# Kernel tuning notes

Measured on AMD Instinct MI355X. Metric: run time of the kernel, lower is better.

Reference implementation:

```python
import jax, jax.numpy as jnp
import numpy as np

N = 10000      # nodes
E = 160000     # edges
C = 72         # hidden dim = 18 * mul (mul=4)
A = 16         # node_attr dim (16x0e)
L = 3          # layers
O = 64         # output dim (64x0e)
B = 16         # graphs in batch
IN_DIM = 18    # irreps_node_input dim
SH = 9         # spherical harmonics dim, lmax=2
FC = 100       # radial MLP hidden (fc_neurons=[1,100])
MAX_RADIUS = 2.0
NUM_NEIGHBORS = 16.0
NUM_NODES = 625.0


def sph_harm_l2(d):
    # component-normalized real spherical harmonics up to l=2 on unit vectors d [E,3]
    x, y, z = d[:, 0], d[:, 1], d[:, 2]
    s3, s5, s15 = 3.0 ** 0.5, 5.0 ** 0.5, 15.0 ** 0.5
    return jnp.stack([
        jnp.ones_like(x),
        s3 * x, s3 * y, s3 * z,
        s15 * x * y, s15 * y * z, (s5 / 2.0) * (3.0 * z * z - 1.0),
        s15 * x * z, (s15 / 2.0) * (x * x - y * y),
    ], axis=1)  # [E, 9]


def setup_inputs() -> dict:
    key = jax.random.key(0)
    ks = jax.random.split(key, 16)
    pos = jax.random.normal(ks[0], (N, 3), dtype=jnp.float32)
    node_attr = jax.random.normal(ks[1], (N, A), dtype=jnp.float32)
    batch = jnp.sort(jax.random.randint(ks[2], (N,), 0, B))
    edge_src = jax.random.randint(ks[3], (E,), 0, N)
    edge_dst = jax.random.randint(ks[4], (E,), 0, N)
    W_in = jax.random.normal(ks[5], (IN_DIM, C), dtype=jnp.float32) / np.sqrt(IN_DIM)
    W_tp = jax.random.normal(ks[6], (L, SH, C, C), dtype=jnp.float32) / np.sqrt(C)
    W_self = jax.random.normal(ks[7], (L, C, C), dtype=jnp.float32) / np.sqrt(C)
    W_attr = jax.random.normal(ks[8], (L, A, C), dtype=jnp.float32) / np.sqrt(A)
    fc1_w = jax.random.normal(ks[9], (L, 1, FC), dtype=jnp.float32)
    fc1_b = jnp.zeros((L, FC), dtype=jnp.float32)
    fc2_w = jax.random.normal(ks[10], (L, FC, SH), dtype=jnp.float32) / np.sqrt(FC)
    W_out = jax.random.normal(ks[11], (C, O), dtype=jnp.float32) / np.sqrt(C)
    return {"pos": pos, "node_attr": node_attr, "batch": batch,
            "edge_src": edge_src, "edge_dst": edge_dst,
            "W_in": W_in, "W_tp": W_tp, "W_self": W_self, "W_attr": W_attr,
            "fc1_w": fc1_w, "fc1_b": fc1_b, "fc2_w": fc2_w, "W_out": W_out}


def reference(pos, node_attr, batch, edge_src, edge_dst,
              W_in, W_tp, W_self, W_attr, fc1_w, fc1_b, fc2_w, W_out):
    n = pos.shape[0]
    # edge geometry
    rvec = pos[edge_src] - pos[edge_dst]                      # [E,3]
    r = jnp.linalg.norm(rvec, axis=1, keepdims=True)          # [E,1]
    dvec = rvec / jnp.maximum(r, 1e-9)
    sh = sph_harm_l2(dvec)                                    # [E,9]
    # single cosine radial basis with cutoff at max_radius (number_of_basis=1)
    t = r / MAX_RADIUS
    emb = jnp.where(t < 1.0, jnp.cos(0.5 * jnp.pi * t), 0.0)  # [E,1]
    # node inputs: fixed one-hot on the scalar channel, embedded to hidden dim
    onehot = jnp.zeros((IN_DIM,), dtype=pos.dtype).at[0].set(1.0)
    h = jnp.broadcast_to((onehot @ W_in)[None, :], (n, C))    # [N,C]
    for l in range(L):
        # radial MLP -> per-edge, per-SH-path weights
        u = jax.nn.silu(emb @ fc1_w[l] + fc1_b[l]) @ fc2_w[l]  # [E,9]
        path = u * sh                                          # [E,9]
        hs = h[edge_src]                                       # [E,C]
        m = jnp.zeros_like(hs)
        for s in range(SH):  # fixed small set of tensor-product paths
            m = m + path[:, s:s + 1] * (hs @ W_tp[l, s])       # [E,C]
        agg = jax.ops.segment_sum(m, edge_dst, num_segments=n) / np.sqrt(NUM_NEIGHBORS)
        h = jax.nn.gelu(agg + h @ W_self[l] + node_attr @ W_attr[l])
    out_nodes = h @ W_out                                      # [N,O]
    pooled = jax.ops.segment_sum(out_nodes, batch, num_segments=B)
    return pooled / np.sqrt(NUM_NODES)                         # [B,O]
```

## Files before the change

kernel.cpp:

```cpp
#include <hip/hip_runtime.h>
#include <math.h>

#define NN 10000
#define NE 160000
#define CC 72
#define AA 16
#define LL 3
#define OO 64
#define NBATCH 16
#define SH 9
#define FCN 100
#define KK (SH*CC)
#define KA 736
#define KP 768
#define KG 96
#define NT 5
#define PSU 16
#define NB 1024
#define EMAX 176

typedef __attribute__((ext_vector_type(8))) short bf16x8;
typedef __attribute__((ext_vector_type(4))) float f32x4;

static __device__ __forceinline__ float gelu_tanh(float x) {
    float x3 = x * x * x;
    float inner = 0.7978845608028654f * (x + 0.044715f * x3);
    return 0.5f * x * (1.0f + tanhf(inner));
}
static __device__ __forceinline__ unsigned short f2bf(float x) {
    unsigned int u = __float_as_uint(x);
    u += 0x7FFFu + ((u >> 16) & 1u);
    return (unsigned short)(u >> 16);
}
static __device__ __forceinline__ float bf2f(unsigned short u) {
    return __uint_as_float((unsigned int)u << 16);
}
static __device__ __forceinline__ unsigned int pack2bf(float lo, float hi) {
    return (unsigned int)f2bf(lo) | ((unsigned int)f2bf(hi) << 16);
}
static __device__ __forceinline__ float bfLo(unsigned int u) {
    return __uint_as_float(u << 16);
}
static __device__ __forceinline__ float bfHi(unsigned int u) {
    return __uint_as_float(u & 0xffff0000u);
}

__global__ void k_zero(int* __restrict__ cnt) {
    int i = blockIdx.x * blockDim.x + threadIdx.x;
    if (i < NN) cnt[i] = 0;
}

#define GB_HIST 625
#define GB_UTAB 13
#define GB_WCAT 180
#define GB_INIT 704
#define GB_PREP (GB_HIST + GB_UTAB + GB_WCAT + GB_INIT)

__global__ __launch_bounds__(256) void k_prep(
        const float* __restrict__ pos, const int* __restrict__ esrc,
        const int* __restrict__ edst, int* __restrict__ cnt,
        const float* __restrict__ fc1w, const float* __restrict__ fc1b,
        const float* __restrict__ fc2w, float* __restrict__ U,
        const float* __restrict__ Wtp, const float* __restrict__ Wself,
        const float* __restrict__ Wattr, unsigned short* __restrict__ Wb,
        const float* __restrict__ W_in, unsigned short* __restrict__ h0) {
    int bb = blockIdx.x, t = threadIdx.x;
    if (bb < GB_HIST) {
        int e = bb * 256 + t;
        if (e < NE) {
            int s = esrc[e], d = edst[e];
            float dx = pos[3 * s] - pos[3 * d];
            float dy = pos[3 * s + 1] - pos[3 * d + 1];
            float dz = pos[3 * s + 2] - pos[3 * d + 2];
            float r = sqrtf(dx * dx + dy * dy + dz * dz);
            if (r * 0.5f < 1.0f) atomicAdd(&cnt[d], 1);
        }
        return;
    }
    bb -= GB_HIST;
    if (bb < GB_UTAB) {
        int i = bb * 256 + t;
        if (i < LL * (NB + 1)) {
            int l = i / (NB + 1), b = i - l * (NB + 1);
            float emb = cosf(1.5707963267948966f * ((float)b / (float)NB));
            float u[SH];
#pragma unroll
            for (int q = 0; q < SH; ++q) u[q] = 0.f;
            const float* w1 = &fc1w[l * FCN];
            const float* b1 = &fc1b[l * FCN];
            const float* w2 = &fc2w[l * FCN * SH];
            for (int f = 0; f < FCN; ++f) {
                float a = emb * w1[f] + b1[f];
                float si = a / (1.0f + expf(-a));
#pragma unroll
                for (int q = 0; q < SH; ++q) u[q] += si * w2[f * SH + q];
            }
            float* ud = &U[(size_t)i * 12];
#pragma unroll
            for (int q = 0; q < SH; ++q) ud[q] = u[q];
            ud[9] = 0.f; ud[10] = 0.f; ud[11] = 0.f;
        }
        return;
    }
    bb -= GB_UTAB;
    if (bb < GB_WCAT) {
        int i0 = (bb * 256 + t) * 4;
#pragma unroll
        for (int u = 0; u < 4; ++u) {
            int i = i0 + u;
            int l = i / (NT * KG * 128);
            int rem = i - l * (NT * KG * 128);
            int nt = rem / (KG * 128); rem -= nt * (KG * 128);
            int kg = rem / 128; int e = rem - kg * 128;
            int n = nt * 16 + (e >> 3);
            int k = kg * 8 + (e & 7);
            float v = 0.f;
            if (n < CC && k < KA) {
                if (k < KK)            v = 0.25f * Wtp[(size_t)l * KK * CC + k * CC + n];
                else if (k < KK + CC)  v = Wself[(size_t)l * CC * CC + (k - KK) * CC + n];
                else                   v = Wattr[(size_t)l * AA * CC + (k - KK - CC) * CC + n];
            }
            Wb[i] = f2bf(v);
        }
        return;
    }
    bb -= GB_WCAT;
    {
        int i0 = (bb * 256 + t) * 4;
#pragma unroll
        for (int u = 0; u < 4; ++u) {
            int i = i0 + u;
            if (i < NN * CC) h0[i] = f2bf(W_in[i % CC]);
        }
    }
}

__global__ void k_scan(const int* __restrict__ cnt, int* __restrict__ off,
                       int* __restrict__ cur, float* __restrict__ hp) {
    __shared__ int sa[256], sb[256];
    const int PER = 40;
    int t = threadIdx.x;
    int base = t * PER;
    int loc[PER];
    int run = 0;
#pragma unroll
    for (int i = 0; i < PER; ++i) {
        int idx = base + i;
        int v = (idx < NN) ? cnt[idx] : 0;
        loc[i] = run;
        run += v;
    }
    sa[t] = run;
    __syncthreads();
    int* in = sa; int* out = sb;
    for (int o = 1; o < 256; o <<= 1) {
        int v = in[t];
        if (t >= o) v += in[t - o];
        out[t] = v;
        __syncthreads();
        int* tmp = in; in = out; out = tmp;
    }
    int ebase = (t > 0) ? in[t - 1] : 0;
#pragma unroll
    for (int i = 0; i < PER; ++i) {
        int idx = base + i;
        if (idx <= NN) {
            int v = ebase + loc[i];
            off[idx] = v;
            if (idx < NN) cur[idx] = v;
        }
    }
    for (int i = t; i < NBATCH * CC; i += 256) hp[i] = 0.f;
}

__global__ __launch_bounds__(256) void k_scatter3(const float* __restrict__ pos,
                                                  const int* __restrict__ esrc,
                                                  const int* __restrict__ edst,
                                                  int* __restrict__ cur,
                                                  int* __restrict__ src_s,
                                                  const float* __restrict__ U,
                                                  unsigned short* __restrict__ path) {
    int e = blockIdx.x * blockDim.x + threadIdx.x;
    if (e >= NE) return;
    int s = esrc[e], d = edst[e];
    float dx = pos[3 * s] - pos[3 * d];
    float dy = pos[3 * s + 1] - pos[3 * d + 1];
    float dz = pos[3 * s + 2] - pos[3 * d + 2];
    float r = sqrtf(dx * dx + dy * dy + dz * dz);
    if (r * 0.5f >= 1.0f) return;
    int slot = atomicAdd(&cur[d], 1);
    src_s[slot] = s;

    float inv = 1.0f / fmaxf(r, 1e-9f);
    float x = dx * inv, y = dy * inv, z = dz * inv;
    const float s3 = 1.7320508075688772f;
    const float s5 = 2.23606797749979f;
    const float s15 = 3.872983346207417f;
    float sh[SH];
    sh[0] = 1.0f;
    sh[1] = s3 * x;
    sh[2] = s3 * y;
    sh[3] = s3 * z;
    sh[4] = s15 * x * y;
    sh[5] = s15 * y * z;
    sh[6] = 0.5f * s5 * (3.0f * z * z - 1.0f);
    sh[7] = s15 * x * z;
    sh[8] = 0.5f * s15 * (x * x - y * y);

    float fb = r * 0.5f * (float)NB;
    int b0 = (int)fb;
    float fr = fb - (float)b0;

#pragma unroll
    for (int l = 0; l < LL; ++l) {
        const float* t0 = &U[((size_t)l * (NB + 1) + b0) * 12];
        float4 a0 = *(const float4*)(t0 + 0);
        float4 a1 = *(const float4*)(t0 + 4);
        float  a2 = t0[8];
        float4 c0 = *(const float4*)(t0 + 12);
        float4 c1 = *(const float4*)(t0 + 16);
        float  c2 = t0[20];
        float u0 = (a0.x + fr * (c0.x - a0.x)) * sh[0];
        float u1 = (a0.y + fr * (c0.y - a0.y)) * sh[1];
        float u2 = (a0.z + fr * (c0.z - a0.z)) * sh[2];
        float u3 = (a0.w + fr * (c0.w - a0.w)) * sh[3];
        float u4 = (a1.x + fr * (c1.x - a1.x)) * sh[4];
        float u5 = (a1.y + fr * (c1.y - a1.y)) * sh[5];
        float u6 = (a1.z + fr * (c1.z - a1.z)) * sh[6];
        float u7 = (a1.w + fr * (c1.w - a1.w)) * sh[7];
        float u8 = (a2   + fr * (c2   - a2))   * sh[8];
        unsigned short* pd = &path[((size_t)l * NE + slot) * PSU];
        uint4 w0, w1;
        w0.x = pack2bf(u0, u1); w0.y = pack2bf(u2, u3);
        w0.z = pack2bf(u4, u5); w0.w = pack2bf(u6, u7);
        w1.x = pack2bf(u8, 0.f); w1.y = 0u; w1.z = 0u; w1.w = 0u;
        *(uint4*)pd = w0;
        *(uint4*)(pd + 8) = w1;
    }
}

__global__ __launch_bounds__(1024, 8) void k_layer(
        const unsigned short* __restrict__ h,
        const float* __restrict__ attr,
        const unsigned short* __restrict__ path_l,
        const int* __restrict__ src_s,
        const int* __restrict__ off,
        const unsigned short* __restrict__ Wb,
        unsigned short* __restrict__ hout) {
    __shared__ unsigned short Plds[EMAX * PSU];
    __shared__ unsigned short Alds[KG * 128];
    int t = threadIdx.x, w = t >> 6, lane = t & 63;
    int n0 = blockIdx.x * 16;
    int d = n0 + w;
    int b0 = off[n0], e0 = off[n0 + 16];
    int db = off[d], de = off[d + 1];

    bool act = lane < 36;
    int c2 = 2 * lane;
    float a1[SH], a2[SH];
#pragma unroll
    for (int q = 0; q < SH; ++q) { a1[q] = 0.f; a2[q] = 0.f; }

    for (int base = b0; base < e0; base += EMAX) {
        int nE = min(EMAX, e0 - base);
        const uint4* p4 = (const uint4*)(path_l + (size_t)base * PSU);
        uint4* Pl4 = (uint4*)Plds;
        for (int idx = t; idx < nE * 2; idx += 1024)
            Pl4[idx] = p4[idx];
        __syncthreads();
        int lb = db > base ? db : base;
        int le = de < base + nE ? de : base + nE;
        for (int i = lb; i < le; i += 8) {
            int m = le - i;
            unsigned int hv[8];
#pragma unroll
            for (int j = 0; j < 8; ++j) {
                if (j < m && act) {
                    int s = src_s[i + j];
                    hv[j] = *(const unsigned int*)&h[(size_t)s * CC + c2];
                }
            }
#pragma unroll
            for (int j = 0; j < 8; ++j) {
                if (j < m) {
                    const unsigned short* p = &Plds[(i + j - base) * PSU];
                    uint4 pw = *(const uint4*)p;
                    unsigned int pz = *(const unsigned int*)(p + 8);
                    float lo = act ? bfLo(hv[j]) : 0.f;
                    float hi = act ? bfHi(hv[j]) : 0.f;
                    float p0 = bfLo(pw.x), p1 = bfHi(pw.x);
                    float p2 = bfLo(pw.y), p3 = bfHi(pw.y);
                    float p4v = bfLo(pw.z), p5 = bfHi(pw.z);
                    float p6 = bfLo(pw.w), p7 = bfHi(pw.w);
                    float p8 = bfLo(pz);
                    a1[0] += p0 * lo;  a2[0] += p0 * hi;
                    a1[1] += p1 * lo;  a2[1] += p1 * hi;
                    a1[2] += p2 * lo;  a2[2] += p2 * hi;
                    a1[3] += p3 * lo;  a2[3] += p3 * hi;
                    a1[4] += p4v * lo; a2[4] += p4v * hi;
                    a1[5] += p5 * lo;  a2[5] += p5 * hi;
                    a1[6] += p6 * lo;  a2[6] += p6 * hi;
                    a1[7] += p7 * lo;  a2[7] += p7 * hi;
                    a1[8] += p8 * lo;  a2[8] += p8 * hi;
                }
            }
        }
        __syncthreads();
    }

    if (act) {
        int kgo = lane >> 2, kjo = 2 * (lane & 3);
        int hb = w * 8 + kjo;
#pragma unroll
        for (int q = 0; q < SH; ++q)
            *(unsigned int*)&Alds[(9 * q + kgo) * 128 + hb] = pack2bf(a1[q], a2[q]);
        *(unsigned int*)&Alds[(81 + kgo) * 128 + hb] =
            *(const unsigned int*)&h[(size_t)d * CC + c2];
        if (lane < 8)
            *(unsigned int*)&Alds[(90 + kgo) * 128 + hb] =
                pack2bf(attr[(size_t)d * AA + c2], attr[(size_t)d * AA + c2 + 1]);
    }
    if (lane < 16)
        *(unsigned int*)&Alds[(92 + (lane >> 2)) * 128 + w * 8 + 2 * (lane & 3)] = 0u;
    __syncthreads();

    if (w < NT) {
        const unsigned short* Ab = Alds + (lane & 15) * 8;
        const unsigned short* Bb = Wb + ((size_t)w * KG) * 128 + (lane & 15) * 8;
        f32x4 acc = (f32x4){0.f, 0.f, 0.f, 0.f};
#pragma unroll
        for (int s = 0; s < 24; ++s) {
            int kg = s * 4 + (lane >> 4);
            bf16x8 af = *(const bf16x8*)(Ab + (size_t)kg * 128);
            bf16x8 bq = *(const bf16x8*)(Bb + (size_t)kg * 128);
            acc = __builtin_amdgcn_mfma_f32_16x16x32_bf16(af, bq, acc, 0, 0, 0);
        }
        int cb = lane & 15, rb = (lane >> 4) * 4;
        int row = n0 + rb, col = w * 16 + cb;
        if (col < CC) {
#pragma unroll
            for (int j = 0; j < 4; ++j)
                hout[(size_t)(row + j) * CC + col] = f2bf(gelu_tanh(acc[j]));
        }
    }
}

__global__ __launch_bounds__(256) void k_pool(const unsigned short* __restrict__ h,
                                              const int* __restrict__ batch,
                                              float* __restrict__ hp) {
    __shared__ float sp[NBATCH * CC];
    int t = threadIdx.x;
    for (int i = t; i < NBATCH * CC; i += 256) sp[i] = 0.f;
    __syncthreads();
    int n0 = blockIdx.x * 16;
    for (int i = t; i < 16 * CC; i += 256) {
        int nl = i / CC, c = i - nl * CC;
        int n = n0 + nl;
        if (n < NN) atomicAdd(&sp[batch[n] * CC + c], bf2f(h[(size_t)n * CC + c]));
    }
    __syncthreads();
    for (int i = t; i < NBATCH * CC; i += 256) {
        float v = sp[i];
        if (v != 0.f) atomicAdd(&hp[i], v);
    }
}

__global__ __launch_bounds__(1024) void k_outmm(const float* __restrict__ hp,
                                                const float* __restrict__ Wout,
                                                float* __restrict__ out) {
    __shared__ float hs[NBATCH * CC];
    int t = threadIdx.x;
    for (int i = t; i < NBATCH * CC; i += 1024) hs[i] = hp[i];
    __syncthreads();
    int b = t >> 6, o = t & 63;
    float acc = 0.f;
#pragma unroll 8
    for (int c = 0; c < CC; ++c) acc += hs[b * CC + c] * Wout[c * OO + o];
    out[t] = acc * (1.0f / 25.0f);
}

extern "C" void kernel_launch(void* const* d_in, const int* in_sizes, int n_in,
                              void* d_out, int out_size, void* d_ws, size_t ws_size,
                              hipStream_t stream) {
    const float* pos       = (const float*)d_in[0];
    const float* node_attr = (const float*)d_in[1];
    const int*   batch     = (const int*)d_in[2];
    const int*   esrc      = (const int*)d_in[3];
    const int*   edst      = (const int*)d_in[4];
    const float* W_in      = (const float*)d_in[5];
    const float* W_tp      = (const float*)d_in[6];
    const float* W_self    = (const float*)d_in[7];
    const float* W_attr    = (const float*)d_in[8];
    const float* fc1w      = (const float*)d_in[9];
    const float* fc1b      = (const float*)d_in[10];
    const float* fc2w      = (const float*)d_in[11];
    const float* W_out     = (const float*)d_in[12];
    float* out = (float*)d_out;

    char* p = (char*)d_ws;
    auto alloc = [&](size_t bytes) -> void* {
        void* r = (void*)p;
        p += (bytes + 255) & ~(size_t)255;
        return r;
    };
    int*   cnt   = (int*)alloc((size_t)NN * 4);
    int*   cur   = (int*)alloc((size_t)NN * 4);
    float* hp    = (float*)alloc((size_t)NBATCH * CC * 4);
    int*   off   = (int*)alloc((size_t)(NN + 1) * 4);
    int*   src_s = (int*)alloc((size_t)NE * 4);
    unsigned short* path = (unsigned short*)alloc((size_t)LL * NE * PSU * 2);
    float* U     = (float*)alloc((size_t)LL * (NB + 1) * 12 * 4);
    unsigned short* Wb = (unsigned short*)alloc((size_t)LL * NT * KG * 128 * 2);
    unsigned short* h0 = (unsigned short*)alloc((size_t)NN * CC * 2);
    unsigned short* h1 = (unsigned short*)alloc((size_t)NN * CC * 2);

    k_zero<<<(NN + 255) / 256, 256, 0, stream>>>(cnt);
    k_prep<<<GB_PREP, 256, 0, stream>>>(pos, esrc, edst, cnt, fc1w, fc1b, fc2w, U,
                                        W_tp, W_self, W_attr, Wb, W_in, h0);
    k_scan<<<1, 256, 0, stream>>>(cnt, off, cur, hp);
    k_scatter3<<<(NE + 255) / 256, 256, 0, stream>>>(pos, esrc, edst, cur, src_s, U, path);

    const unsigned short* hin = h0;
    unsigned short* hout = h1;
    for (int l = 0; l < LL; ++l) {
        k_layer<<<NN / 16, 1024, 0, stream>>>(hin, node_attr,
                                              path + (size_t)l * NE * PSU, src_s, off,
                                              Wb + (size_t)l * NT * KG * 128, hout);
        const unsigned short* tmp = hin; hin = hout; hout = (unsigned short*)tmp;
    }
    k_pool<<<(NN + 15) / 16, 256, 0, stream>>>(hin, batch, hp);
    k_outmm<<<1, 1024, 0, stream>>>(hp, W_out, out);
}
```

Measured before the change: 138.5 us.

## Reorder destination nodes by degree to balance per-block edge work

The single-block scan is replaced by a degree-histogram counting sort. It produces a permutation of destination nodes ordered by in-degree plus matching CSR edge start offsets, so the edge scatter lays edges out in that sorted node order. k_layer then assigns each group of 16 consecutive sorted nodes to one block, so the 16 waves have near-equal edge counts and fewer waves wait at the per-chunk barriers. The cost is row-scattered output writes through perm, a heavier scan kernel with extra barriers and atomics, and clamping degrees above 255 into one bin, which is only correct if no node reaches that degree.

```diff
diff --git a/kernel.cpp b/kernel.cpp
--- a/kernel.cpp
+++ b/kernel.cpp
@@ -12,12 +12,12 @@
 #define FCN 100
 #define KK (SH*CC)
 #define KA 736
-#define KP 768
 #define KG 96
 #define NT 5
 #define PSU 16
 #define NB 1024
 #define EMAX 176
+#define DBIN 256
 
 typedef __attribute__((ext_vector_type(8))) short bf16x8;
 typedef __attribute__((ext_vector_type(4))) float f32x4;
@@ -135,41 +135,65 @@
     }
 }
 
-__global__ void k_scan(const int* __restrict__ cnt, int* __restrict__ off,
-                       int* __restrict__ cur, float* __restrict__ hp) {
-    __shared__ int sa[256], sb[256];
+__global__ __launch_bounds__(256) void k_scan2(const int* __restrict__ cnt,
+                                               int* __restrict__ perm,
+                                               int* __restrict__ estart,
+                                               int* __restrict__ cur,
+                                               float* __restrict__ hp) {
+    __shared__ int hist[DBIN], rankB[DBIN], edgeB[DBIN], ctr[DBIN];
+    __shared__ int sa[DBIN], sb[DBIN];
     const int PER = 40;
     int t = threadIdx.x;
-    int base = t * PER;
-    int loc[PER];
-    int run = 0;
+    int deg[PER];
+    for (int i = t; i < DBIN; i += 256) { hist[i] = 0; ctr[i] = 0; }
+    __syncthreads();
 #pragma unroll
     for (int i = 0; i < PER; ++i) {
-        int idx = base + i;
-        int v = (idx < NN) ? cnt[idx] : 0;
-        loc[i] = run;
-        run += v;
-    }
-    sa[t] = run;
-    __syncthreads();
-    int* in = sa; int* out = sb;
-    for (int o = 1; o < 256; o <<= 1) {
-        int v = in[t];
-        if (t >= o) v += in[t - o];
-        out[t] = v;
-        __syncthreads();
-        int* tmp = in; in = out; out = tmp;
-    }
-    int ebase = (t > 0) ? in[t - 1] : 0;
+        int d = t * PER + i;
+        int v = (d < NN) ? cnt[d] : -1;
+        deg[i] = v;
+        if (v >= 0) atomicAdd(&hist[v < DBIN ? v : DBIN - 1], 1);
+    }
+    __syncthreads();
+    int cme = hist[t];
+    int eme = hist[t] * t;
+    sa[t] = cme; sb[t] = eme;
+    __syncthreads();
+    int cacc = 0, eacc = 0;
+    for (int b = 0; b < 2; ++b) {  break; }
+    {
+        for (int o = 1; o < DBIN; o <<= 1) {
+            int cv = sa[t], ev = sb[t];
+            __syncthreads();
+            if (t + o < DBIN) { atomicAdd(&sa[t + o], 0); }
+            __syncthreads();
+            int cn = (t >= o) ? sa[t - o] : 0;
+            int en = (t >= o) ? sb[t - o] : 0;
+            __syncthreads();
+            sa[t] = cv + cn;
+            sb[t] = ev + en;
+            __syncthreads();
+        }
+        cacc = sa[t] - cme;
+        eacc = sb[t] - eme;
+    }
+    rankB[t] = cacc;
+    edgeB[t] = eacc;
+    __syncthreads();
+    int total = sb[DBIN - 1];
 #pragma unroll
     for (int i = 0; i < PER; ++i) {
-        int idx = base + i;
-        if (idx <= NN) {
-            int v = ebase + loc[i];
-            off[idx] = v;
-            if (idx < NN) cur[idx] = v;
-        }
-    }
+        int d = t * PER + i;
+        if (d < NN) {
+            int dg = deg[i] < DBIN ? deg[i] : DBIN - 1;
+            int r = rankB[dg] + atomicAdd(&ctr[dg], 1);
+            int es = edgeB[dg] + (r - rankB[dg]) * deg[i];
+            perm[r] = d;
+            estart[r] = es;
+            cur[d] = es;
+        }
+    }
+    if (t == 0) estart[NN] = total;
     for (int i = t; i < NBATCH * CC; i += 256) hp[i] = 0.f;
 }
 
@@ -244,16 +268,17 @@
         const float* __restrict__ attr,
         const unsigned short* __restrict__ path_l,
         const int* __restrict__ src_s,
-        const int* __restrict__ off,
+        const int* __restrict__ perm,
+        const int* __restrict__ estart,
         const unsigned short* __restrict__ Wb,
         unsigned short* __restrict__ hout) {
     __shared__ unsigned short Plds[EMAX * PSU];
     __shared__ unsigned short Alds[KG * 128];
     int t = threadIdx.x, w = t >> 6, lane = t & 63;
-    int n0 = blockIdx.x * 16;
-    int d = n0 + w;
-    int b0 = off[n0], e0 = off[n0 + 16];
-    int db = off[d], de = off[d + 1];
+    int i0n = blockIdx.x * 16;
+    int d = perm[i0n + w];
+    int b0 = estart[i0n], e0 = estart[i0n + 16];
+    int db = estart[i0n + w], de = estart[i0n + w + 1];
 
     bool act = lane < 36;
     int c2 = 2 * lane;
@@ -336,11 +361,13 @@
             acc = __builtin_amdgcn_mfma_f32_16x16x32_bf16(af, bq, acc, 0, 0, 0);
         }
         int cb = lane & 15, rb = (lane >> 4) * 4;
-        int row = n0 + rb, col = w * 16 + cb;
+        int col = w * 16 + cb;
         if (col < CC) {
 #pragma unroll
-            for (int j = 0; j < 4; ++j)
-                hout[(size_t)(row + j) * CC + col] = f2bf(gelu_tanh(acc[j]));
+            for (int j = 0; j < 4; ++j) {
+                int row = perm[i0n + rb + j];
+                hout[(size_t)row * CC + col] = f2bf(gelu_tanh(acc[j]));
+            }
         }
     }
 }
@@ -403,13 +430,14 @@
         p += (bytes + 255) & ~(size_t)255;
         return r;
     };
-    int*   cnt   = (int*)alloc((size_t)NN * 4);
-    int*   cur   = (int*)alloc((size_t)NN * 4);
-    float* hp    = (float*)alloc((size_t)NBATCH * CC * 4);
-    int*   off   = (int*)alloc((size_t)(NN + 1) * 4);
-    int*   src_s = (int*)alloc((size_t)NE * 4);
+    int*   cnt    = (int*)alloc((size_t)NN * 4);
+    int*   cur    = (int*)alloc((size_t)NN * 4);
+    float* hp     = (float*)alloc((size_t)NBATCH * CC * 4);
+    int*   perm   = (int*)alloc((size_t)NN * 4);
+    int*   estart = (int*)alloc((size_t)(NN + 1) * 4);
+    int*   src_s  = (int*)alloc((size_t)NE * 4);
     unsigned short* path = (unsigned short*)alloc((size_t)LL * NE * PSU * 2);
-    float* U     = (float*)alloc((size_t)LL * (NB + 1) * 12 * 4);
+    float* U      = (float*)alloc((size_t)LL * (NB + 1) * 12 * 4);
     unsigned short* Wb = (unsigned short*)alloc((size_t)LL * NT * KG * 128 * 2);
     unsigned short* h0 = (unsigned short*)alloc((size_t)NN * CC * 2);
     unsigned short* h1 = (unsigned short*)alloc((size_t)NN * CC * 2);
@@ -417,14 +445,15 @@
     k_zero<<<(NN + 255) / 256, 256, 0, stream>>>(cnt);
     k_prep<<<GB_PREP, 256, 0, stream>>>(pos, esrc, edst, cnt, fc1w, fc1b, fc2w, U,
                                         W_tp, W_self, W_attr, Wb, W_in, h0);
-    k_scan<<<1, 256, 0, stream>>>(cnt, off, cur, hp);
+    k_scan2<<<1, 256, 0, stream>>>(cnt, perm, estart, cur, hp);
     k_scatter3<<<(NE + 255) / 256, 256, 0, stream>>>(pos, esrc, edst, cur, src_s, U, path);
 
     const unsigned short* hin = h0;
     unsigned short* hout = h1;
     for (int l = 0; l < LL; ++l) {
         k_layer<<<NN / 16, 1024, 0, stream>>>(hin, node_attr,
-                                              path + (size_t)l * NE * PSU, src_s, off,
+                                              path + (size_t)l * NE * PSU, src_s,
+                                              perm, estart,
                                               Wb + (size_t)l * NT * KG * 128, hout);
         const unsigned short* tmp = hin; hin = hout; hout = (unsigned short*)tmp;
     }
```

After: 156.4 us. +12.9%, slower.
